# Kernel optimization log

Measured on AMD Instinct MI355X. Metric: run time of the kernel, lower is better.

## Reference

```python
import jax, jax.numpy as jnp
import numpy as np

CHUNK = 32  # chunk_size in _delta_rule_chunkwise

def _l2norm(x, eps=1e-6):
    return x * jax.lax.rsqrt(jnp.sum(x * x, axis=-1, keepdims=True) + eps)

def setup_inputs() -> dict:
    key = jax.random.key(0)
    kq, kk, kv, kb = jax.random.split(key, 4)
    b, h, L, dk, dv = 2, 8, 4096, 128, 128
    return {
        "q": jax.random.normal(kq, (b, h, L, dk), jnp.float32),
        "k": jax.random.normal(kk, (b, h, L, dk), jnp.float32),
        "v": jax.random.normal(kv, (b, h, L, dv), jnp.float32),
        "beta": jax.random.uniform(kb, (b, h, L), jnp.float32),  # sigmoid(b_proj) in (0,1)
    }

def _delta_rule_chunkwise(q, k, v, beta, chunk_size=CHUNK):
    b, h, L, dk = q.shape
    dv = v.shape[-1]
    c = chunk_size
    pad = (-L) % c
    if pad:
        q = jnp.pad(q, ((0, 0), (0, 0), (0, pad), (0, 0)))
        k = jnp.pad(k, ((0, 0), (0, 0), (0, pad), (0, 0)))
        v = jnp.pad(v, ((0, 0), (0, 0), (0, pad), (0, 0)))
        beta = jnp.pad(beta, ((0, 0), (0, 0), (0, pad)))
    n = (L + pad) // c
    q = _l2norm(q)
    k = _l2norm(k)
    v = v * beta[..., None]
    k_beta = k * beta[..., None]
    # [b,h,n,c,d]
    resh = lambda t: t.reshape(b, h, n, c, t.shape[-1])
    q, k, v, k_beta = map(resh, (q, k, v, k_beta))
    # strictly-lower-triangular -(k_beta k^T)
    lower = jnp.tril(jnp.ones((c, c), bool), -1)
    att = -(k_beta @ jnp.swapaxes(k, -1, -2)) * lower
    # forward substitution: invert (I - A) for strictly lower A (unrolled, c=32 static)
    for i in range(1, c):
        upd = jnp.einsum('...j,...jm->...m', att[..., i, :], att[..., :, :i])
        att = att.at[..., i, :i].add(upd)
    att = att + jnp.eye(c, dtype=att.dtype)
    att = att.astype(jnp.bfloat16).astype(q.dtype)  # matches .to(torch.bfloat16)
    u = att @ v         # [b,h,n,c,dv]
    w = att @ k_beta    # [b,h,n,c,dk]
    future = jnp.triu(jnp.ones((c, c), bool), 1)
    S0 = jnp.zeros((b, h, dk, dv), q.dtype)

    def step(S, inp):
        q_i, k_i, u_i, w_i = inp  # [b,h,c,d]
        att_local = jnp.where(future, 0.0, q_i @ jnp.swapaxes(k_i, -1, -2))
        u_new = u_i - w_i @ S
        o_i = q_i @ S + att_local @ u_new
        S_new = S + jnp.swapaxes(k_i, -1, -2) @ u_new
        return S_new, o_i

    xs = tuple(jnp.moveaxis(t, 2, 0) for t in (q, k, u, w))  # scan over chunks
    S, o = jax.lax.scan(step, S0, xs)
    o = jnp.moveaxis(o, 0, 2).reshape(b, h, n * c, dv)[:, :, :L]
    return o, S

def reference(q, k, v, beta):
    return _delta_rule_chunkwise(q, k, v, beta)
```

## Files before the change

kernel.cpp:

```cpp
#include <hip/hip_runtime.h>
#include <hip/hip_bf16.h>


#define B 2
#define H 8
#define LSEQ 4096
#define DK 128
#define DV 128
#define C 32
#define NCHUNK (LSEQ / C)
#define BH (B * H)
#define NBLK (BH * NCHUNK)
#define NG 16
#define GSZ 8

typedef _Float16 f16x8 __attribute__((ext_vector_type(8)));
typedef float f32x4 __attribute__((ext_vector_type(4)));

union U4H8 { uint4 u; f16x8 h; };

__device__ inline unsigned short f2h(float f) {
    _Float16 h = (_Float16)f;
    unsigned short u;
    __builtin_memcpy(&u, &h, 2);
    return u;
}
__device__ inline float h2f(unsigned int v) {
    unsigned short s = (unsigned short)v;
    _Float16 h;
    __builtin_memcpy(&h, &s, 2);
    return (float)h;
}
__device__ inline unsigned int pack2(float a, float b) {
    return (unsigned int)f2h(a) | ((unsigned int)f2h(b) << 16);
}
__device__ inline float dot4(float4 a, float4 b) {
    return a.x * b.x + a.y * b.y + a.z * b.z + a.w * b.w;
}
__device__ inline float bf16r(float x) {
    return __bfloat162float(__float2bfloat16(x));
}
__device__ inline uint2 pk4(float v0, float v1, float v2, float v3) {
    uint2 p; p.x = pack2(v0, v1); p.y = pack2(v2, v3); return p;
}
__device__ inline f32x4 up4(uint2 p) {
    f32x4 v;
    v[0] = h2f(p.x & 0xffffu); v[1] = h2f(p.x >> 16);
    v[2] = h2f(p.y & 0xffffu); v[3] = h2f(p.y >> 16);
    return v;
}

#define S40 40
#define S136 136

__global__ __launch_bounds__(64) void phase2_kernel(
    const float* __restrict__ qg, const float* __restrict__ kg,
    const float* __restrict__ vg, const float* __restrict__ betag,
    uint4* __restrict__ wnegf, uint4* __restrict__ qnf,
    uint4* __restrict__ ktf, uint4* __restrict__ atf,
    uint2* __restrict__ uf)
{
    __shared__ alignas(16) _Float16 sA [32 * S40];
    __shared__ alignas(16) _Float16 sAT[32 * S40];
    __shared__ alignas(16) _Float16 sTT[32 * S40];
    __shared__ alignas(16) _Float16 sTB[32 * S40];
    __shared__ alignas(16) _Float16 sW [32 * S136];
    __shared__ alignas(16) float sbetaL[32];
    __shared__ alignas(16) float skscL[32];

    const int l = threadIdx.x;
    const int lm = l & 15, qd = l >> 4;
    const int blk = blockIdx.x;
    const long tb = (long)blk * C * DK;
    const f32x4 z4 = {0.f, 0.f, 0.f, 0.f};

    if (l < 32) sbetaL[l] = betag[(long)blk * C + l];

    U4H8 qF[8], kF[8];
    float ssq[2] = {0.f, 0.f}, ssk[2] = {0.f, 0.f};
    #pragma unroll
    for (int mt = 0; mt < 2; mt++) {
        #pragma unroll
        for (int kt = 0; kt < 4; kt++) {
            const float* qp = qg + tb + (long)(mt * 16 + lm) * DK + kt * 32 + qd * 8;
            const float* kp = kg + tb + (long)(mt * 16 + lm) * DK + kt * 32 + qd * 8;
            float4 a0 = *(const float4*)qp, a1 = *(const float4*)(qp + 4);
            float4 b0 = *(const float4*)kp, b1 = *(const float4*)(kp + 4);
            ssq[mt] += dot4(a0, a0) + dot4(a1, a1);
            ssk[mt] += dot4(b0, b0) + dot4(b1, b1);
            U4H8 x;
            x.u.x = pack2(a0.x, a0.y); x.u.y = pack2(a0.z, a0.w);
            x.u.z = pack2(a1.x, a1.y); x.u.w = pack2(a1.z, a1.w);
            qF[mt * 4 + kt] = x;
            U4H8 y;
            y.u.x = pack2(b0.x, b0.y); y.u.y = pack2(b0.z, b0.w);
            y.u.z = pack2(b1.x, b1.y); y.u.w = pack2(b1.z, b1.w);
            kF[mt * 4 + kt] = y;
        }
    }
    float qsc[2], ksc[2];
    #pragma unroll
    for (int mt = 0; mt < 2; mt++) {
        float s = ssq[mt];
        s += __shfl_xor(s, 16, 64);
        s += __shfl_xor(s, 32, 64);
        qsc[mt] = rsqrtf(s + 1e-6f);
        float t = ssk[mt];
        t += __shfl_xor(t, 16, 64);
        t += __shfl_xor(t, 32, 64);
        ksc[mt] = rsqrtf(t + 1e-6f);
    }
    if (qd == 0) { skscL[lm] = ksc[0]; skscL[16 + lm] = ksc[1]; }

    f32x4 alT[3] = {z4, z4, z4};
    #pragma unroll
    for (int kt = 0; kt < 4; kt++) {
        alT[0] = __builtin_amdgcn_mfma_f32_16x16x32_f16(kF[kt].h,     qF[kt].h,     alT[0], 0, 0, 0);
        alT[1] = __builtin_amdgcn_mfma_f32_16x16x32_f16(kF[kt].h,     qF[4 + kt].h, alT[1], 0, 0, 0);
        alT[2] = __builtin_amdgcn_mfma_f32_16x16x32_f16(kF[4 + kt].h, qF[4 + kt].h, alT[2], 0, 0, 0);
    }
    #pragma unroll
    for (int mt = 0; mt < 2; mt++) {
        _Float16 qs = (_Float16)qsc[mt];
        #pragma unroll
        for (int kt = 0; kt < 4; kt++) {
            U4H8 x;
            x.h = qF[mt * 4 + kt].h * qs;
            qnf[((long)blk * 8 + mt * 4 + kt) * 64 + l] = x.u;
        }
    }
    f32x4 rw[4] = {z4, z4, z4, z4};
    #pragma unroll
    for (int kt = 0; kt < 4; kt++) {
        rw[0] = __builtin_amdgcn_mfma_f32_16x16x32_f16(kF[kt].h,     kF[kt].h,     rw[0], 0, 0, 0);
        rw[1] = __builtin_amdgcn_mfma_f32_16x16x32_f16(kF[kt].h,     kF[4 + kt].h, rw[1], 0, 0, 0);
        rw[2] = __builtin_amdgcn_mfma_f32_16x16x32_f16(kF[4 + kt].h, kF[kt].h,     rw[2], 0, 0, 0);
        rw[3] = __builtin_amdgcn_mfma_f32_16x16x32_f16(kF[4 + kt].h, kF[4 + kt].h, rw[3], 0, 0, 0);
    }

    float4 b4[2], ks4[2];
    b4[0]  = *(const float4*)&sbetaL[qd * 4];      b4[1]  = *(const float4*)&sbetaL[16 + qd * 4];
    ks4[0] = *(const float4*)&skscL[qd * 4];       ks4[1] = *(const float4*)&skscL[16 + qd * 4];
    const float bcol0 = sbetaL[lm], bcol1 = sbetaL[16 + lm];

    {
        *(uint2*)&sTB[lm * S40 + 16 + qd * 4] = (uint2){0u, 0u};
        float v[4];
        #pragma unroll
        for (int r = 0; r < 4; r++) {
            int c = qd * 4 + r;
            v[r] = (c <= lm) ? (qsc[0] * (&ks4[0].x)[r] * alT[0][r]) : 0.f;
        }
        *(uint2*)&sTB[lm * S40 + qd * 4] = pk4(v[0], v[1], v[2], v[3]);
        #pragma unroll
        for (int r = 0; r < 4; r++) v[r] = qsc[1] * (&ks4[0].x)[r] * alT[1][r];
        *(uint2*)&sTB[(16 + lm) * S40 + qd * 4] = pk4(v[0], v[1], v[2], v[3]);
        #pragma unroll
        for (int r = 0; r < 4; r++) {
            int c = qd * 4 + r;
            v[r] = (c <= lm) ? (qsc[1] * (&ks4[1].x)[r] * alT[2][r]) : 0.f;
        }
        *(uint2*)&sTB[(16 + lm) * S40 + 16 + qd * 4] = pk4(v[0], v[1], v[2], v[3]);
    }
    #pragma unroll
    for (int f = 0; f < 2; f++) {
        uint4 x = *(const uint4*)&sTB[(f * 16 + lm) * S40 + qd * 8];
        atf[((long)blk * 2 + f) * 64 + l] = x;
    }

    {
        float v[4];
        *(uint2*)&sA [lm * S40 + 16 + qd * 4]        = (uint2){0u, 0u};
        *(uint2*)&sAT[(16 + lm) * S40 + qd * 4]      = (uint2){0u, 0u};
        *(uint2*)&sTT[(16 + lm) * S40 + qd * 4]      = (uint2){0u, 0u};
        #pragma unroll
        for (int r = 0; r < 4; r++) {
            int c = qd * 4 + r;
            v[r] = (c < lm) ? (-bcol0 * ksc[0] * (&ks4[0].x)[r] * rw[0][r]) : 0.f;
        }
        *(uint2*)&sA[lm * S40 + qd * 4] = pk4(v[0], v[1], v[2], v[3]);
        #pragma unroll
        for (int r = 0; r < 4; r++) v[r] = -bcol1 * ksc[1] * (&ks4[0].x)[r] * rw[1][r];
        *(uint2*)&sA[(16 + lm) * S40 + qd * 4] = pk4(v[0], v[1], v[2], v[3]);
        #pragma unroll
        for (int r = 0; r < 4; r++) {
            int c = qd * 4 + r;
            v[r] = (c < lm) ? (-bcol1 * ksc[1] * (&ks4[1].x)[r] * rw[3][r]) : 0.f;
        }
        *(uint2*)&sA[(16 + lm) * S40 + 16 + qd * 4] = pk4(v[0], v[1], v[2], v[3]);
        #pragma unroll
        for (int r = 0; r < 4; r++) {
            int c = qd * 4 + r;
            v[r] = (c > lm) ? (-(&b4[0].x)[r] * (&ks4[0].x)[r] * ksc[0] * rw[0][r]) : 0.f;
        }
        *(uint2*)&sAT[lm * S40 + qd * 4] = pk4(v[0], v[1], v[2], v[3]);
        #pragma unroll
        for (int r = 0; r < 4; r++) v[r] = -(&b4[1].x)[r] * (&ks4[1].x)[r] * ksc[0] * rw[2][r];
        *(uint2*)&sAT[lm * S40 + 16 + qd * 4] = pk4(v[0], v[1], v[2], v[3]);
        #pragma unroll
        for (int r = 0; r < 4; r++) {
            int c = qd * 4 + r;
            v[r] = (c > lm) ? (-(&b4[1].x)[r] * (&ks4[1].x)[r] * ksc[1] * rw[3][r]) : 0.f;
        }
        *(uint2*)&sAT[(16 + lm) * S40 + 16 + qd * 4] = pk4(v[0], v[1], v[2], v[3]);
        #pragma unroll
        for (int r = 0; r < 4; r++) {
            int c = qd * 4 + r;
            v[r] = (c > lm) ? (-(&b4[0].x)[r] * (&ks4[0].x)[r] * ksc[0] * rw[0][r])
                            : ((c == lm) ? 1.0f : 0.f);
        }
        *(uint2*)&sTT[lm * S40 + qd * 4] = pk4(v[0], v[1], v[2], v[3]);
        #pragma unroll
        for (int r = 0; r < 4; r++) v[r] = -(&b4[1].x)[r] * (&ks4[1].x)[r] * ksc[0] * rw[2][r];
        *(uint2*)&sTT[lm * S40 + 16 + qd * 4] = pk4(v[0], v[1], v[2], v[3]);
        #pragma unroll
        for (int r = 0; r < 4; r++) {
            int c = qd * 4 + r;
            v[r] = (c > lm) ? (-(&b4[1].x)[r] * (&ks4[1].x)[r] * ksc[1] * rw[3][r])
                            : ((c == lm) ? 1.0f : 0.f);
        }
        *(uint2*)&sTT[(16 + lm) * S40 + 16 + qd * 4] = pk4(v[0], v[1], v[2], v[3]);
    }
    f32x4 Tc[3], TTc[3];
    #pragma unroll
    for (int r = 0; r < 4; r++) {
        int rr = qd * 4 + r;
        Tc[0][r] = (lm < rr) ? (-(&b4[0].x)[r] * (&ks4[0].x)[r] * ksc[0] * rw[0][r])
                             : ((lm == rr) ? 1.0f : 0.f);
        Tc[1][r] = -(&b4[1].x)[r] * (&ks4[1].x)[r] * ksc[0] * rw[2][r];
        Tc[2][r] = (lm < rr) ? (-(&b4[1].x)[r] * (&ks4[1].x)[r] * ksc[1] * rw[3][r])
                             : ((lm == rr) ? 1.0f : 0.f);
        TTc[0][r] = (rr < lm) ? (-bcol0 * ksc[0] * (&ks4[0].x)[r] * rw[0][r])
                              : ((rr == lm) ? 1.0f : 0.f);
        TTc[1][r] = -bcol1 * ksc[1] * (&ks4[0].x)[r] * rw[1][r];
        TTc[2][r] = (rr < lm) ? (-bcol1 * ksc[1] * (&ks4[1].x)[r] * rw[3][r])
                              : ((rr == lm) ? 1.0f : 0.f);
    }

    #pragma unroll
    for (int p = 0; p < 4; p++) {
        U4H8 AF[2], ATF[2], TTF[2];
        AF[0].u  = *(const uint4*)&sA [lm * S40 + qd * 8];
        AF[1].u  = *(const uint4*)&sA [(16 + lm) * S40 + qd * 8];
        ATF[0].u = *(const uint4*)&sAT[lm * S40 + qd * 8];
        ATF[1].u = *(const uint4*)&sAT[(16 + lm) * S40 + qd * 8];
        TTF[0].u = *(const uint4*)&sTT[lm * S40 + qd * 8];
        TTF[1].u = *(const uint4*)&sTT[(16 + lm) * S40 + qd * 8];

        f32x4 A2_00 = __builtin_amdgcn_mfma_f32_16x16x32_f16(AF[0].h, ATF[0].h, z4, 0, 0, 0);
        f32x4 A2_10 = __builtin_amdgcn_mfma_f32_16x16x32_f16(AF[1].h, ATF[0].h, z4, 0, 0, 0);
        f32x4 A2_11 = __builtin_amdgcn_mfma_f32_16x16x32_f16(AF[1].h, ATF[1].h, z4, 0, 0, 0);
        f32x4 A2T_00 = __builtin_amdgcn_mfma_f32_16x16x32_f16(ATF[0].h, AF[0].h, z4, 0, 0, 0);
        f32x4 A2T_01 = __builtin_amdgcn_mfma_f32_16x16x32_f16(ATF[0].h, AF[1].h, z4, 0, 0, 0);
        f32x4 A2T_11 = __builtin_amdgcn_mfma_f32_16x16x32_f16(ATF[1].h, AF[1].h, z4, 0, 0, 0);

        {
            float v[4];
            #pragma unroll
            for (int r = 0; r < 4; r++) { int c = qd * 4 + r; v[r] = (c < lm) ? A2T_00[r] : 0.f; }
            *(uint2*)&sA[lm * S40 + qd * 4] = pk4(v[0], v[1], v[2], v[3]);
            *(uint2*)&sA[(16 + lm) * S40 + qd * 4] = pk4(A2T_01[0], A2T_01[1], A2T_01[2], A2T_01[3]);
            #pragma unroll
            for (int r = 0; r < 4; r++) { int c = qd * 4 + r; v[r] = (c < lm) ? A2T_11[r] : 0.f; }
            *(uint2*)&sA[(16 + lm) * S40 + 16 + qd * 4] = pk4(v[0], v[1], v[2], v[3]);
        }
        if (p < 3) {
            float v[4];
            #pragma unroll
            for (int r = 0; r < 4; r++) { int c = qd * 4 + r; v[r] = (c > lm) ? A2_00[r] : 0.f; }
            *(uint2*)&sAT[lm * S40 + qd * 4] = pk4(v[0], v[1], v[2], v[3]);
            *(uint2*)&sAT[lm * S40 + 16 + qd * 4] = pk4(A2_10[0], A2_10[1], A2_10[2], A2_10[3]);
            #pragma unroll
            for (int r = 0; r < 4; r++) { int c = qd * 4 + r; v[r] = (c > lm) ? A2_11[r] : 0.f; }
            *(uint2*)&sAT[(16 + lm) * S40 + 16 + qd * 4] = pk4(v[0], v[1], v[2], v[3]);
        }
        U4H8 AnF[2];
        AnF[0].u = *(const uint4*)&sA[lm * S40 + qd * 8];
        AnF[1].u = *(const uint4*)&sA[(16 + lm) * S40 + qd * 8];
        Tc[0]  = __builtin_amdgcn_mfma_f32_16x16x32_f16(AnF[0].h, TTF[0].h, Tc[0], 0, 0, 0);
        Tc[1]  = __builtin_amdgcn_mfma_f32_16x16x32_f16(AnF[1].h, TTF[0].h, Tc[1], 0, 0, 0);
        Tc[2]  = __builtin_amdgcn_mfma_f32_16x16x32_f16(AnF[1].h, TTF[1].h, Tc[2], 0, 0, 0);
        TTc[0] = __builtin_amdgcn_mfma_f32_16x16x32_f16(TTF[0].h, AnF[0].h, TTc[0], 0, 0, 0);
        TTc[1] = __builtin_amdgcn_mfma_f32_16x16x32_f16(TTF[0].h, AnF[1].h, TTc[1], 0, 0, 0);
        TTc[2] = __builtin_amdgcn_mfma_f32_16x16x32_f16(TTF[1].h, AnF[1].h, TTc[2], 0, 0, 0);
        if (p < 3) {
            *(uint2*)&sTT[lm * S40 + qd * 4]             = pk4(Tc[0][0], Tc[0][1], Tc[0][2], Tc[0][3]);
            *(uint2*)&sTT[lm * S40 + 16 + qd * 4]        = pk4(Tc[1][0], Tc[1][1], Tc[1][2], Tc[1][3]);
            *(uint2*)&sTT[(16 + lm) * S40 + 16 + qd * 4] = pk4(Tc[2][0], Tc[2][1], Tc[2][2], Tc[2][3]);
        }
    }

    {
        *(uint2*)&sTB[lm * S40 + 16 + qd * 4] = (uint2){0u, 0u};
        float v[4];
        #pragma unroll
        for (int r = 0; r < 4; r++) v[r] = bf16r(TTc[0][r]) * (&b4[0].x)[r];
        *(uint2*)&sTB[lm * S40 + qd * 4] = pk4(v[0], v[1], v[2], v[3]);
        #pragma unroll
        for (int r = 0; r < 4; r++) v[r] = bf16r(TTc[1][r]) * (&b4[0].x)[r];
        *(uint2*)&sTB[(16 + lm) * S40 + qd * 4] = pk4(v[0], v[1], v[2], v[3]);
        #pragma unroll
        for (int r = 0; r < 4; r++) v[r] = bf16r(TTc[2][r]) * (&b4[1].x)[r];
        *(uint2*)&sTB[(16 + lm) * S40 + 16 + qd * 4] = pk4(v[0], v[1], v[2], v[3]);
    }
    U4H8 TbF[2];
    TbF[0].u = *(const uint4*)&sTB[lm * S40 + qd * 8];
    TbF[1].u = *(const uint4*)&sTB[(16 + lm) * S40 + qd * 8];

    float kscj[8];
    #pragma unroll
    for (int j = 0; j < 8; j++) kscj[j] = skscL[qd * 8 + j];
    #pragma unroll
    for (int nt = 0; nt < 8; nt++) {
        U4H8 bV, bK;
        #pragma unroll
        for (int j = 0; j < 8; j++) {
            const long ro = tb + (long)(qd * 8 + j) * DK + nt * 16 + lm;
            bV.h[j] = (_Float16)vg[ro];
            bK.h[j] = (_Float16)(kg[ro] * kscj[j]);
        }
        ktf[((long)blk * 8 + nt) * 64 + l] = bK.u;
        f32x4 u0 = __builtin_amdgcn_mfma_f32_16x16x32_f16(TbF[0].h, bV.h, z4, 0, 0, 0);
        f32x4 u1 = __builtin_amdgcn_mfma_f32_16x16x32_f16(TbF[1].h, bV.h, z4, 0, 0, 0);
        uf[(((long)blk * 2 + 0) * 8 + nt) * 64 + l] = pk4(u0[0], u0[1], u0[2], u0[3]);
        uf[(((long)blk * 2 + 1) * 8 + nt) * 64 + l] = pk4(u1[0], u1[1], u1[2], u1[3]);
        f32x4 w0 = __builtin_amdgcn_mfma_f32_16x16x32_f16(TbF[0].h, bK.h, z4, 0, 0, 0);
        f32x4 w1 = __builtin_amdgcn_mfma_f32_16x16x32_f16(TbF[1].h, bK.h, z4, 0, 0, 0);
        #pragma unroll
        for (int r = 0; r < 4; r++) {
            sW[(qd * 4 + r) * S136 + nt * 16 + lm]        = (_Float16)(-w0[r]);
            sW[(16 + qd * 4 + r) * S136 + nt * 16 + lm]   = (_Float16)(-w1[r]);
        }
    }
    #pragma unroll
    for (int mt2 = 0; mt2 < 2; mt2++) {
        #pragma unroll
        for (int kt = 0; kt < 4; kt++) {
            uint4 x = *(const uint4*)&sW[(mt2 * 16 + lm) * S136 + kt * 32 + qd * 8];
            wnegf[((long)blk * 8 + mt2 * 4 + kt) * 64 + l] = x;
        }
    }
}

__global__ __launch_bounds__(64, 2) void phase3a_kernel(
    const uint4* __restrict__ wnegf, const uint4* __restrict__ ktf,
    const uint2* __restrict__ uf,
    uint4* __restrict__ Pf, uint2* __restrict__ Qgf)
{
    __shared__ alignas(16) _Float16 S16[16 * 16 * 8];
    __shared__ alignas(16) _Float16 U16[4 * 16 * 8];
    __shared__ alignas(16) _Float16 PT[128 * 16];

    const int l = threadIdx.x;
    const int lm = l & 15, quad = l >> 4;
    const int idx = blockIdx.x;
    const int s = idx >> 8;
    const int g = idx & 255;
    const int mode = s >> 3;
    const int w = s & 7;
    const int bh = g >> 4;
    const int grp = g & 15;
    const f32x4 z4 = {0.f, 0.f, 0.f, 0.f};

    if (mode && grp == 0) return;

    f32x4 accS[8];
    #pragma unroll
    for (int mt = 0; mt < 8; mt++) {
        #pragma unroll
        for (int r = 0; r < 4; r++)
            accS[mt][r] = (mode && mt == w && quad * 4 + r == lm) ? 1.f : 0.f;
    }

    struct FragA { uint4 aW[2][4]; uint4 aK[8]; uint2 aU[2]; };
    FragA fA, fB;

    auto loadf = [&](FragA& f, int t) {
        const long blk = (long)bh * NCHUNK + grp * GSZ + t;
        #pragma unroll
        for (int mt2 = 0; mt2 < 2; mt2++)
            #pragma unroll
            for (int kt = 0; kt < 4; kt++)
                f.aW[mt2][kt] = wnegf[(blk * 8 + mt2 * 4 + kt) * 64 + l];
        #pragma unroll
        for (int mt = 0; mt < 8; mt++) f.aK[mt] = ktf[(blk * 8 + mt) * 64 + l];
        if (!mode) {
            #pragma unroll
            for (int mt2 = 0; mt2 < 2; mt2++)
                f.aU[mt2] = uf[((blk * 2 + mt2) * 8 + w) * 64 + l];
        }
    };

    auto compute = [&](const FragA& f) {
        #pragma unroll
        for (int mt = 0; mt < 8; mt++) {
            int g2 = 2 * mt + (quad >> 1);
            int sub = (quad & 1) * 4;
            *(uint2*)&S16[(g2 * 16 + lm) * 8 + sub] =
                pk4(accS[mt][0], accS[mt][1], accS[mt][2], accS[mt][3]);
        }
        f32x4 accU[2];
        #pragma unroll
        for (int mt2 = 0; mt2 < 2; mt2++)
            accU[mt2] = mode ? z4 : up4(f.aU[mt2]);
        #pragma unroll
        for (int kt = 0; kt < 4; kt++) {
            U4H8 bs;
            bs.u = *(const uint4*)&S16[((kt * 4 + quad) * 16 + lm) * 8];
            #pragma unroll
            for (int mt2 = 0; mt2 < 2; mt2++) {
                U4H8 aw; aw.u = f.aW[mt2][kt];
                accU[mt2] = __builtin_amdgcn_mfma_f32_16x16x32_f16(aw.h, bs.h, accU[mt2], 0, 0, 0);
            }
        }
        #pragma unroll
        for (int mt2 = 0; mt2 < 2; mt2++) {
            int g2 = 2 * mt2 + (quad >> 1);
            int sub = (quad & 1) * 4;
            *(uint2*)&U16[(g2 * 16 + lm) * 8 + sub] =
                pk4(accU[mt2][0], accU[mt2][1], accU[mt2][2], accU[mt2][3]);
        }
        U4H8 bu;
        bu.u = *(const uint4*)&U16[(quad * 16 + lm) * 8];
        #pragma unroll
        for (int mt = 0; mt < 8; mt++) {
            U4H8 ak; ak.u = f.aK[mt];
            accS[mt] = __builtin_amdgcn_mfma_f32_16x16x32_f16(ak.h, bu.h, accS[mt], 0, 0, 0);
        }
    };

    loadf(fA, 0);
    #pragma unroll 1
    for (int t = 0; t < GSZ; t += 2) {
        loadf(fB, t + 1);
        compute(fA);
        if (t + 2 < GSZ) loadf(fA, t + 2);
        compute(fB);
    }

    if (!mode) {
        const long qb = (((long)(bh * NG + grp)) * 8 + w) * 8 * 64;
        #pragma unroll
        for (int mt = 0; mt < 8; mt++)
            Qgf[qb + mt * 64 + l] = pk4(accS[mt][0], accS[mt][1], accS[mt][2], accS[mt][3]);
    } else {
        #pragma unroll
        for (int mt = 0; mt < 8; mt++)
            #pragma unroll
            for (int r = 0; r < 4; r++)
                PT[(mt * 16 + quad * 4 + r) * 16 + lm] = (_Float16)accS[mt][r];
        const int tl = ((w & 1) << 5) | (l & 31);
        const int half = l >> 5;
        const long pb = ((long)(bh * NG + grp)) * 8;
        #pragma unroll
        for (int i = 0; i < 4; i++) {
            int mt = half * 4 + i;
            uint4 x = *(const uint4*)&PT[(mt * 16 + (tl & 15)) * 16 + ((tl >> 4) & 1) * 8];
            Pf[((pb + mt) * 4 + (w >> 1)) * 64 + tl] = x;
        }
    }
}

__global__ __launch_bounds__(256, 1) void phase3b_kernel(
    const uint4* __restrict__ Pf, const uint2* __restrict__ Qgf,
    uint2* __restrict__ Sjf, float* __restrict__ S_out)
{
    __shared__ alignas(16) _Float16 S16[2][16 * 16 * 8];

    const int tid = threadIdx.x;
    const int l = tid & 63;
    const int ww = tid >> 6;
    const int lm = l & 15, quad = l >> 4;
    const int bh = blockIdx.x & 15;
    const int w = blockIdx.x >> 4;

    f32x4 accS[2];
    #pragma unroll
    for (int i = 0; i < 2; i++) accS[i] = (f32x4){0.f, 0.f, 0.f, 0.f};

    uint2 Q0[2], Q1[2];
    uint4 P0[2][4], P1[2][4];

    auto loadQ = [&](uint2 (&Q)[2], int j) {
        const long b = (((long)(bh * NG + j)) * 8 + w) * 8 * 64;
        #pragma unroll
        for (int i = 0; i < 2; i++) Q[i] = Qgf[b + (ww * 2 + i) * 64 + l];
    };
    auto loadP = [&](uint4 (&P)[2][4], int j) {
        const long b = ((long)(bh * NG + j)) * 8;
        #pragma unroll
        for (int i = 0; i < 2; i++)
            #pragma unroll
            for (int kt = 0; kt < 4; kt++)
                P[i][kt] = Pf[((b + ww * 2 + i) * 4 + kt) * 64 + l];
    };
    auto computeB = [&](int j, const uint2 (&Q)[2], const uint4 (&P)[2][4]) {
        f32x4 ns[2];
        #pragma unroll
        for (int i = 0; i < 2; i++) ns[i] = up4(Q[i]);
        if (j) {
            const int buf = j & 1;
            #pragma unroll
            for (int i = 0; i < 2; i++) {
                int mt = ww * 2 + i;
                int g2 = 2 * mt + (quad >> 1);
                int sub = (quad & 1) * 4;
                *(uint2*)&S16[buf][(g2 * 16 + lm) * 8 + sub] =
                    pk4(accS[i][0], accS[i][1], accS[i][2], accS[i][3]);
            }
            __syncthreads();
            #pragma unroll
            for (int kt = 0; kt < 4; kt++) {
                U4H8 bs;
                bs.u = *(const uint4*)&S16[buf][((kt * 4 + quad) * 16 + lm) * 8];
                #pragma unroll
                for (int i = 0; i < 2; i++) {
                    U4H8 ap; ap.u = P[i][kt];
                    ns[i] = __builtin_amdgcn_mfma_f32_16x16x32_f16(ap.h, bs.h, ns[i], 0, 0, 0);
                }
            }
        }
        #pragma unroll
        for (int i = 0; i < 2; i++) accS[i] = ns[i];
        if (j < 15) {
            const long sb = (((long)(bh * 16 + (j + 1))) * 8 + w) * 8 * 64;
            #pragma unroll
            for (int i = 0; i < 2; i++)
                Sjf[sb + (ww * 2 + i) * 64 + l] = pk4(ns[i][0], ns[i][1], ns[i][2], ns[i][3]);
        } else {
            #pragma unroll
            for (int i = 0; i < 2; i++) {
                int mt = ww * 2 + i;
                #pragma unroll
                for (int r = 0; r < 4; r++)
                    S_out[(long)bh * (DK * DV) + (long)(mt * 16 + quad * 4 + r) * DV + w * 16 + lm] = ns[i][r];
            }
        }
    };

    loadQ(Q0, 0);
    loadP(P1, 1);
    #pragma unroll 1
    for (int j = 0; j < 16; j += 2) {
        loadQ(Q1, j + 1);
        computeB(j, Q0, P0);
        if (j + 2 < 16) { loadP(P0, j + 2); loadQ(Q0, j + 2); }
        computeB(j + 1, Q1, P1);
        if (j + 3 < 16) loadP(P1, j + 3);
    }
}

struct Frags {
    uint4 aW[2][4];
    uint4 aQ[2][4];
    uint4 aK[8];
    uint4 aAt[2];
    uint2 aU[2];
};

__global__ __launch_bounds__(64, 1) void phase3c_kernel(
    const uint4* __restrict__ wnegf, const uint4* __restrict__ qnf,
    const uint4* __restrict__ ktf, const uint4* __restrict__ atf,
    const uint2* __restrict__ uf, const uint2* __restrict__ Sjf,
    float* __restrict__ o_out)
{
    __shared__ alignas(16) _Float16 S16[16 * 16 * 8];
    __shared__ alignas(16) _Float16 U16[4 * 16 * 8];

    const int l = threadIdx.x;
    const int lm = l & 15, quad = l >> 4;
    const int idx = blockIdx.x;
    const int w = idx >> 8;
    const int g = idx & 255;
    const int bh = g >> 4;
    const int grp = g & 15;
    const int dv = w * 16 + lm;

    f32x4 accS[8];
    if (grp == 0) {
        #pragma unroll
        for (int mt = 0; mt < 8; mt++) accS[mt] = (f32x4){0.f, 0.f, 0.f, 0.f};
    } else {
        const long sb = (((long)(bh * 16 + grp)) * 8 + w) * 8 * 64;
        #pragma unroll
        for (int mt = 0; mt < 8; mt++) accS[mt] = up4(Sjf[sb + mt * 64 + l]);
    }

    auto loadf = [&](Frags& f, int t) {
        const long blk = (long)bh * NCHUNK + grp * GSZ + t;
        #pragma unroll
        for (int mt2 = 0; mt2 < 2; mt2++) {
            #pragma unroll
            for (int kt = 0; kt < 4; kt++) {
                f.aW[mt2][kt] = wnegf[(blk * 8 + mt2 * 4 + kt) * 64 + l];
                f.aQ[mt2][kt] = qnf[(blk * 8 + mt2 * 4 + kt) * 64 + l];
            }
            f.aAt[mt2] = atf[(blk * 2 + mt2) * 64 + l];
            f.aU[mt2] = uf[((blk * 2 + mt2) * 8 + w) * 64 + l];
        }
        #pragma unroll
        for (int mt = 0; mt < 8; mt++) f.aK[mt] = ktf[(blk * 8 + mt) * 64 + l];
    };

    auto compute = [&](const Frags& f, int t) {
        #pragma unroll
        for (int mt = 0; mt < 8; mt++) {
            int g2 = 2 * mt + (quad >> 1);
            int sub = (quad & 1) * 4;
            *(uint2*)&S16[(g2 * 16 + lm) * 8 + sub] =
                pk4(accS[mt][0], accS[mt][1], accS[mt][2], accS[mt][3]);
        }
        f32x4 accU[2], accO[2];
        #pragma unroll
        for (int mt2 = 0; mt2 < 2; mt2++) {
            accU[mt2] = up4(f.aU[mt2]);
            accO[mt2] = (f32x4){0.f, 0.f, 0.f, 0.f};
        }
        #pragma unroll
        for (int kt = 0; kt < 4; kt++) {
            U4H8 bs;
            bs.u = *(const uint4*)&S16[((kt * 4 + quad) * 16 + lm) * 8];
            #pragma unroll
            for (int mt2 = 0; mt2 < 2; mt2++) {
                U4H8 aw, aq;
                aw.u = f.aW[mt2][kt];
                aq.u = f.aQ[mt2][kt];
                accU[mt2] = __builtin_amdgcn_mfma_f32_16x16x32_f16(aw.h, bs.h, accU[mt2], 0, 0, 0);
                accO[mt2] = __builtin_amdgcn_mfma_f32_16x16x32_f16(aq.h, bs.h, accO[mt2], 0, 0, 0);
            }
        }
        #pragma unroll
        for (int mt2 = 0; mt2 < 2; mt2++) {
            int g2 = 2 * mt2 + (quad >> 1);
            int sub = (quad & 1) * 4;
            *(uint2*)&U16[(g2 * 16 + lm) * 8 + sub] =
                pk4(accU[mt2][0], accU[mt2][1], accU[mt2][2], accU[mt2][3]);
        }
        U4H8 bu;
        bu.u = *(const uint4*)&U16[(quad * 16 + lm) * 8];
        const long ob = ((long)bh * LSEQ + (long)(grp * GSZ + t) * C) * DV;
        #pragma unroll
        for (int mt2 = 0; mt2 < 2; mt2++) {
            U4H8 aa;
            aa.u = f.aAt[mt2];
            accO[mt2] = __builtin_amdgcn_mfma_f32_16x16x32_f16(aa.h, bu.h, accO[mt2], 0, 0, 0);
            #pragma unroll
            for (int r = 0; r < 4; r++)
                o_out[ob + (long)(mt2 * 16 + quad * 4 + r) * DV + dv] = accO[mt2][r];
        }
        #pragma unroll
        for (int mt = 0; mt < 8; mt++) {
            U4H8 ak;
            ak.u = f.aK[mt];
            accS[mt] = __builtin_amdgcn_mfma_f32_16x16x32_f16(ak.h, bu.h, accS[mt], 0, 0, 0);
        }
    };

    Frags fA, fB;
    loadf(fA, 0);
    #pragma unroll 1
    for (int t = 0; t < GSZ; t += 2) {
        loadf(fB, t + 1);
        compute(fA, t);
        if (t + 2 < GSZ) loadf(fA, t + 2);
        compute(fB, t + 1);
    }
}

extern "C" void kernel_launch(void* const* d_in, const int* in_sizes, int n_in,
                              void* d_out, int out_size, void* d_ws, size_t ws_size,
                              hipStream_t stream) {
    const float* q    = (const float*)d_in[0];
    const float* k    = (const float*)d_in[1];
    const float* v    = (const float*)d_in[2];
    const float* beta = (const float*)d_in[3];

    float* o = (float*)d_out;
    float* S = o + (long)BH * LSEQ * DV;

    const size_t nwq = (size_t)NBLK * 8 * 64;
    uint4* wnegf = (uint4*)d_ws;
    uint4* qnf = wnegf + nwq;
    uint4* ktf = qnf + nwq;
    uint4* atf = ktf + nwq;
    uint2* uf  = (uint2*)(atf + (size_t)NBLK * 2 * 64);
    uint4* Pf  = (uint4*)(uf + (size_t)NBLK * 16 * 64);
    uint2* Qgf = (uint2*)(Pf + (size_t)BH * NG * 8 * 4 * 64);
    uint2* Sjf = Qgf + (size_t)BH * NG * 8 * 8 * 64;

    phase2_kernel<<<NBLK, 64, 0, stream>>>(q, k, v, beta, wnegf, qnf, ktf, atf, uf);
    phase3a_kernel<<<16 * 256, 64, 0, stream>>>(wnegf, ktf, uf, Pf, Qgf);
    phase3b_kernel<<<BH * 8, 256, 0, stream>>>(Pf, Qgf, Sjf, S);
    phase3c_kernel<<<8 * 256, 64, 0, stream>>>(wnegf, qnf, ktf, atf, uf, Sjf, o);
}
```

Before: 217.5 us.

## Split phase3c chunk work across two wavefronts per block

Each phase3c block now runs two 64-lane wavefronts instead of one. Each wave handles half of the output rows (one 16-row tile) and half of the state tiles, so per-wave fragment registers and MFMA chains shrink and the kernel gets twice as many waves to hide memory latency. The waves share the fp16 state and U tiles through LDS, which adds two block barriers per chunk step.

```diff
diff --git a/kernel.cpp b/kernel.cpp
--- a/kernel.cpp
+++ b/kernel.cpp
@@ -550,15 +550,15 @@
     }
 }
 
-struct Frags {
-    uint4 aW[2][4];
-    uint4 aQ[2][4];
-    uint4 aK[8];
-    uint4 aAt[2];
-    uint2 aU[2];
+struct Frag2 {
+    uint4 aW[4];
+    uint4 aQ[4];
+    uint4 aK[4];
+    uint4 aAt;
+    uint2 aU;
 };
 
-__global__ __launch_bounds__(64, 1) void phase3c_kernel(
+__global__ __launch_bounds__(128, 1) void phase3c_kernel(
     const uint4* __restrict__ wnegf, const uint4* __restrict__ qnf,
     const uint4* __restrict__ ktf, const uint4* __restrict__ atf,
     const uint2* __restrict__ uf, const uint2* __restrict__ Sjf,
@@ -567,7 +567,9 @@
     __shared__ alignas(16) _Float16 S16[16 * 16 * 8];
     __shared__ alignas(16) _Float16 U16[4 * 16 * 8];
 
-    const int l = threadIdx.x;
+    const int tid = threadIdx.x;
+    const int l = tid & 63;
+    const int ww = tid >> 6;
     const int lm = l & 15, quad = l >> 4;
     const int idx = blockIdx.x;
     const int w = idx >> 8;
@@ -576,87 +578,76 @@
     const int grp = g & 15;
     const int dv = w * 16 + lm;
 
-    f32x4 accS[8];
+    f32x4 accS[4];
     if (grp == 0) {
         #pragma unroll
-        for (int mt = 0; mt < 8; mt++) accS[mt] = (f32x4){0.f, 0.f, 0.f, 0.f};
+        for (int i = 0; i < 4; i++) accS[i] = (f32x4){0.f, 0.f, 0.f, 0.f};
     } else {
         const long sb = (((long)(bh * 16 + grp)) * 8 + w) * 8 * 64;
         #pragma unroll
-        for (int mt = 0; mt < 8; mt++) accS[mt] = up4(Sjf[sb + mt * 64 + l]);
-    }
-
-    auto loadf = [&](Frags& f, int t) {
+        for (int i = 0; i < 4; i++) accS[i] = up4(Sjf[sb + (ww * 4 + i) * 64 + l]);
+    }
+
+    auto loadf = [&](Frag2& f, int t) {
         const long blk = (long)bh * NCHUNK + grp * GSZ + t;
         #pragma unroll
-        for (int mt2 = 0; mt2 < 2; mt2++) {
-            #pragma unroll
-            for (int kt = 0; kt < 4; kt++) {
-                f.aW[mt2][kt] = wnegf[(blk * 8 + mt2 * 4 + kt) * 64 + l];
-                f.aQ[mt2][kt] = qnf[(blk * 8 + mt2 * 4 + kt) * 64 + l];
-            }
-            f.aAt[mt2] = atf[(blk * 2 + mt2) * 64 + l];
-            f.aU[mt2] = uf[((blk * 2 + mt2) * 8 + w) * 64 + l];
-        }
-        #pragma unroll
-        for (int mt = 0; mt < 8; mt++) f.aK[mt] = ktf[(blk * 8 + mt) * 64 + l];
+        for (int kt = 0; kt < 4; kt++) {
+            f.aW[kt] = wnegf[(blk * 8 + ww * 4 + kt) * 64 + l];
+            f.aQ[kt] = qnf[(blk * 8 + ww * 4 + kt) * 64 + l];
+        }
+        f.aAt = atf[(blk * 2 + ww) * 64 + l];
+        f.aU = uf[((blk * 2 + ww) * 8 + w) * 64 + l];
+        #pragma unroll
+        for (int i = 0; i < 4; i++) f.aK[i] = ktf[(blk * 8 + ww * 4 + i) * 64 + l];
     };
 
-    auto compute = [&](const Frags& f, int t) {
-        #pragma unroll
-        for (int mt = 0; mt < 8; mt++) {
+    auto compute = [&](const Frag2& f, int t) {
+        #pragma unroll
+        for (int i = 0; i < 4; i++) {
+            int mt = ww * 4 + i;
             int g2 = 2 * mt + (quad >> 1);
             int sub = (quad & 1) * 4;
             *(uint2*)&S16[(g2 * 16 + lm) * 8 + sub] =
-                pk4(accS[mt][0], accS[mt][1], accS[mt][2], accS[mt][3]);
-        }
-        f32x4 accU[2], accO[2];
-        #pragma unroll
-        for (int mt2 = 0; mt2 < 2; mt2++) {
-            accU[mt2] = up4(f.aU[mt2]);
-            accO[mt2] = (f32x4){0.f, 0.f, 0.f, 0.f};
-        }
+                pk4(accS[i][0], accS[i][1], accS[i][2], accS[i][3]);
+        }
+        __syncthreads();
+        f32x4 accU = up4(f.aU);
+        f32x4 accO = (f32x4){0.f, 0.f, 0.f, 0.f};
         #pragma unroll
         for (int kt = 0; kt < 4; kt++) {
             U4H8 bs;
             bs.u = *(const uint4*)&S16[((kt * 4 + quad) * 16 + lm) * 8];
-            #pragma unroll
-            for (int mt2 = 0; mt2 < 2; mt2++) {
-                U4H8 aw, aq;
-                aw.u = f.aW[mt2][kt];
-                aq.u = f.aQ[mt2][kt];
-                accU[mt2] = __builtin_amdgcn_mfma_f32_16x16x32_f16(aw.h, bs.h, accU[mt2], 0, 0, 0);
-                accO[mt2] = __builtin_amdgcn_mfma_f32_16x16x32_f16(aq.h, bs.h, accO[mt2], 0, 0, 0);
-            }
-        }
-        #pragma unroll
-        for (int mt2 = 0; mt2 < 2; mt2++) {
-            int g2 = 2 * mt2 + (quad >> 1);
+            U4H8 aw, aq;
+            aw.u = f.aW[kt];
+            aq.u = f.aQ[kt];
+            accU = __builtin_amdgcn_mfma_f32_16x16x32_f16(aw.h, bs.h, accU, 0, 0, 0);
+            accO = __builtin_amdgcn_mfma_f32_16x16x32_f16(aq.h, bs.h, accO, 0, 0, 0);
+        }
+        {
+            int g2 = 2 * ww + (quad >> 1);
             int sub = (quad & 1) * 4;
             *(uint2*)&U16[(g2 * 16 + lm) * 8 + sub] =
-                pk4(accU[mt2][0], accU[mt2][1], accU[mt2][2], accU[mt2][3]);
-        }
+                pk4(accU[0], accU[1], accU[2], accU[3]);
+        }
+        __syncthreads();
         U4H8 bu;
         bu.u = *(const uint4*)&U16[(quad * 16 + lm) * 8];
         const long ob = ((long)bh * LSEQ + (long)(grp * GSZ + t) * C) * DV;
-        #pragma unroll
-        for (int mt2 = 0; mt2 < 2; mt2++) {
-            U4H8 aa;
-            aa.u = f.aAt[mt2];
-            accO[mt2] = __builtin_amdgcn_mfma_f32_16x16x32_f16(aa.h, bu.h, accO[mt2], 0, 0, 0);
-            #pragma unroll
-            for (int r = 0; r < 4; r++)
-                o_out[ob + (long)(mt2 * 16 + quad * 4 + r) * DV + dv] = accO[mt2][r];
-        }
-        #pragma unroll
-        for (int mt = 0; mt < 8; mt++) {
+        U4H8 aa;
+        aa.u = f.aAt;
+        accO = __builtin_amdgcn_mfma_f32_16x16x32_f16(aa.h, bu.h, accO, 0, 0, 0);
+        #pragma unroll
+        for (int r = 0; r < 4; r++)
+            o_out[ob + (long)(ww * 16 + quad * 4 + r) * DV + dv] = accO[r];
+        #pragma unroll
+        for (int i = 0; i < 4; i++) {
             U4H8 ak;
-            ak.u = f.aK[mt];
-            accS[mt] = __builtin_amdgcn_mfma_f32_16x16x32_f16(ak.h, bu.h, accS[mt], 0, 0, 0);
+            ak.u = f.aK[i];
+            accS[i] = __builtin_amdgcn_mfma_f32_16x16x32_f16(ak.h, bu.h, accS[i], 0, 0, 0);
         }
     };
 
-    Frags fA, fB;
+    Frag2 fA, fB;
     loadf(fA, 0);
     #pragma unroll 1
     for (int t = 0; t < GSZ; t += 2) {
@@ -691,5 +682,5 @@
     phase2_kernel<<<NBLK, 64, 0, stream>>>(q, k, v, beta, wnegf, qnf, ktf, atf, uf);
     phase3a_kernel<<<16 * 256, 64, 0, stream>>>(wnegf, ktf, uf, Pf, Qgf);
     phase3b_kernel<<<BH * 8, 256, 0, stream>>>(Pf, Qgf, Sjf, S);
-    phase3c_kernel<<<8 * 256, 64, 0, stream>>>(wnegf, qnf, ktf, atf, uf, Sjf, o);
-}
+    phase3c_kernel<<<8 * 256, 128, 0, stream>>>(wnegf, qnf, ktf, atf, uf, Sjf, o);
+}
```

Measured after the change: 234.1 us. +7.6%, slower.
